# Kernel optimization log

Measured on AMD Instinct MI355X. Metric: run time of the kernel, lower is better.

Reference implementation:

```python
import jax, jax.numpy as jnp
import numpy as np

B, CQ, CKV, H, W = 8, 128, 64, 64, 64
DIM = CQ // 8  # qk_reduction=8 -> 16


def conv1x1(x, w, b):
    # x: [B, Cin, H, W], w: [Cout, Cin], b: [Cout]
    return jnp.einsum('bchw,oc->bohw', x, w) + b[None, :, None, None]


def setup_inputs() -> dict:
    key = jax.random.key(0)
    ks = jax.random.split(key, 12)
    s = 0.05
    return {
        'x4q': jax.random.normal(ks[0], (B, CQ, H, W), jnp.float32),
        'x4kv': jax.random.normal(ks[1], (B, CKV, H, W), jnp.float32),
        'Wq': jax.random.normal(ks[2], (DIM, CQ), jnp.float32) * s,
        'bq': jax.random.normal(ks[3], (DIM,), jnp.float32) * s,
        'Wk': jax.random.normal(ks[4], (DIM, CKV), jnp.float32) * s,
        'bk': jax.random.normal(ks[5], (DIM,), jnp.float32) * s,
        'Wv': jax.random.normal(ks[6], (CQ, CKV), jnp.float32) * s,
        'bv': jax.random.normal(ks[7], (CQ,), jnp.float32) * s,
        'Wo': jax.random.normal(ks[8], (CQ, CQ), jnp.float32) * s,
        'bo': jax.random.normal(ks[9], (CQ,), jnp.float32) * s,
        'gamma': jax.random.normal(ks[10], (1,), jnp.float32) * s,
    }


def reference(x4q, x4kv, Wq, bq, Wk, bk, Wv, bv, Wo, bo, gamma):
    q = conv1x1(x4q, Wq, bq)    # [B, DIM, H, W]
    k = conv1x1(x4kv, Wk, bk)   # [B, DIM, H, W]
    v = conv1x1(x4kv, Wv, bv)   # [B, CQ,  H, W]
    b, dim, h_, w_ = q.shape
    n = h_ * w_
    qf = q.reshape(b, dim, n)
    kf = k.reshape(b, dim, n)
    vf = v.reshape(b, -1, n)
    # score[b, n_query, m_key] = q^T k, scaled by dim^-0.5
    score = jnp.einsum('bdn,bdm->bnm', qf, kf) * (float(dim) ** -0.5)
    attention = jax.nn.softmax(score, axis=2)          # over keys m
    hmat = jnp.einsum('bcm,bnm->bcn', vf, attention)   # bmm(v, att^T)
    hmap = hmat.reshape(b, -1, h_, w_)
    hmap = conv1x1(hmap, Wo, bo)
    return gamma * hmap + x4q
```

## Files before the change

kernel.cpp:

```cpp
#include <hip/hip_runtime.h>

#define NB 8
#define CQ 128
#define CKV 64
#define NPIX 4096
#define QDIM 16
#define KVBLK 128
#define NTI (NPIX / KVBLK)

typedef float f32x4 __attribute__((ext_vector_type(4)));
typedef float f32x16 __attribute__((ext_vector_type(16)));
typedef __bf16 bf16x8 __attribute__((ext_vector_type(8)));
typedef unsigned short u16;
typedef u16 u16x4 __attribute__((ext_vector_type(4)));
typedef u16 u16x8 __attribute__((ext_vector_type(8)));
typedef unsigned int u32;
typedef u32 u32x2 __attribute__((ext_vector_type(2)));
typedef u32 u32x4 __attribute__((ext_vector_type(4)));

static __device__ __forceinline__ u16 f2bf(float f) {
  unsigned int u = __builtin_bit_cast(unsigned int, f);
  u = (u + 0x7FFFu + ((u >> 16) & 1u)) >> 16;
  return (u16)u;
}
static __device__ __forceinline__ u32 cvtpk(float lo, float hi) {
  u32 r; asm("v_cvt_pk_bf16_f32 %0, %1, %2" : "=v"(r) : "v"(lo), "v"(hi)); return r;
}
static __device__ __forceinline__ void plswap(u32& a, u32& b) {
#if __has_builtin(__builtin_amdgcn_permlane32_swap)
  u32x2 r = __builtin_amdgcn_permlane32_swap(a, b, false, false);
  a = r[0]; b = r[1];
#else
  asm volatile("v_permlane32_swap_b32 %0, %1" : "+v"(a), "+v"(b));
#endif
}
static __device__ __forceinline__ void gload_lds16(const void* g, void* l) {
  __builtin_amdgcn_global_load_lds((const __attribute__((address_space(1))) void*)g,
                                   (__attribute__((address_space(3))) void*)l, 16, 0, 0);
}

__global__ __launch_bounds__(256) void proj_qkv(
    const float* __restrict__ xq, const float* __restrict__ Wq, const float* __restrict__ bq,
    const float* __restrict__ xkv, const float* __restrict__ Wk, const float* __restrict__ bk,
    const float* __restrict__ Wv, const float* __restrict__ bv,
    u16* __restrict__ Qs, u16* __restrict__ Ks, u16* __restrict__ Vt)
{
  __shared__ __align__(16) char smem[50688];
  int t = threadIdx.x;
  if ((int)blockIdx.x < NB * 64) {
    int bid = (int)blockIdx.x;
    float (*wq)[CQ]        = (float(*)[CQ])smem;
    float (*wk)[CKV]       = (float(*)[CKV])(smem + 8192);
    float (*redq)[64][17]  = (float(*)[64][17])(smem + 12288);
    float (*redk)[64][17]  = (float(*)[64][17])(smem + 29696);
    for (int i = t; i < QDIM * CQ; i += 256) wq[i >> 7][i & 127] = Wq[i];
    for (int i = t; i < QDIM * CKV; i += 256) wk[i >> 6][i & 63] = Wk[i];
    __syncthreads();
    int b = bid >> 6;
    int n0 = (bid & 63) << 6;
    int px = t & 63, cg = t >> 6;
    int n = n0 + px;
    const float* xqp = xq + (size_t)b * CQ * NPIX + n;
    const float* xkp = xkv + (size_t)b * CKV * NPIX + n;
    float qa[QDIM], ka[QDIM];
    #pragma unroll
    for (int d = 0; d < QDIM; d++) { qa[d] = 0.f; ka[d] = 0.f; }
    int cq0 = cg * 32, ck0 = cg * 16;
    #pragma unroll 4
    for (int c = cq0; c < cq0 + 32; c++) {
      float x = xqp[(size_t)c * NPIX];
      #pragma unroll
      for (int d = 0; d < QDIM; d++) qa[d] = fmaf(wq[d][c], x, qa[d]);
    }
    #pragma unroll 4
    for (int c = ck0; c < ck0 + 16; c++) {
      float x = xkp[(size_t)c * NPIX];
      #pragma unroll
      for (int d = 0; d < QDIM; d++) ka[d] = fmaf(wk[d][c], x, ka[d]);
    }
    #pragma unroll
    for (int d = 0; d < QDIM; d++) { redq[cg][px][d] = qa[d]; redk[cg][px][d] = ka[d]; }
    __syncthreads();
    const float SC = 0.25f * 1.44269504088896340736f;
    int d0 = cg * 4;
    u16x4 oq, ok;
    #pragma unroll
    for (int j = 0; j < 4; j++) {
      float sq = redq[0][px][d0 + j] + redq[1][px][d0 + j]
               + redq[2][px][d0 + j] + redq[3][px][d0 + j] + bq[d0 + j];
      oq[j] = f2bf(sq * SC);
      float sk = redk[0][px][d0 + j] + redk[1][px][d0 + j]
               + redk[2][px][d0 + j] + redk[3][px][d0 + j] + bk[d0 + j];
      ok[j] = f2bf(sk);
    }
    size_t o = ((size_t)b * NPIX + n) * QDIM + d0;
    *(u16x4*)(Qs + o) = oq;
    *(u16x4*)(Ks + o) = ok;
  } else {
    int bid = (int)blockIdx.x - NB * 64;
    float (*wv)[CKV + 1] = (float(*)[CKV + 1])smem;
    float (*xs)[64 + 4]  = (float(*)[64 + 4])(smem + 33280);
    int b = bid >> 6;
    int n0 = (bid & 63) << 6;
    for (int i = t; i < CQ * CKV; i += 256) wv[i >> 6][i & 63] = Wv[i];
    const float* xp = xkv + (size_t)b * CKV * NPIX + n0;
    for (int i = t; i < CKV * 16; i += 256) {
      int c = i >> 4, c4 = (i & 15) * 4;
      *(f32x4*)(&xs[c][c4]) = *(const f32x4*)(xp + (size_t)c * NPIX + c4);
    }
    __syncthreads();
    int cog = t >> 4, pg = t & 15;
    int co0 = cog * 8, p0 = pg * 4;
    float acc[8][4];
    #pragma unroll
    for (int j = 0; j < 8; j++) {
      float bb = bv[co0 + j];
      #pragma unroll
      for (int p = 0; p < 4; p++) acc[j][p] = bb;
    }
    #pragma unroll 2
    for (int c = 0; c < CKV; c++) {
      float xv[4];
      #pragma unroll
      for (int p = 0; p < 4; p++) xv[p] = xs[c][p0 + p];
      #pragma unroll
      for (int j = 0; j < 8; j++) {
        float wvv = wv[co0 + j][c];
        #pragma unroll
        for (int p = 0; p < 4; p++) acc[j][p] = fmaf(wvv, xv[p], acc[j][p]);
      }
    }
    #pragma unroll
    for (int j = 0; j < 8; j++) {
      u16x4 ov;
      #pragma unroll
      for (int p = 0; p < 4; p++) ov[p] = f2bf(acc[j][p]);
      *(u16x4*)(Vt + ((size_t)b * CQ + co0 + j) * NPIX + n0 + p0) = ov;
    }
  }
}

__global__ __launch_bounds__(256, 2) void attn(
    const u16* __restrict__ Qs, const u16* __restrict__ Ks, const u16* __restrict__ Vt,
    const float* __restrict__ Wo, const float* __restrict__ bo,
    const float* __restrict__ gamma, const float* __restrict__ xq,
    float* __restrict__ out)
{
  __shared__ u16 v_s[2][128][128];
  __shared__ float d_red[2][2][32];
  __shared__ float d_x[2][32];
  __shared__ float d_inv[2][32];
  __shared__ float bos[128];

  int t = (int)threadIdx.x;
  int w = t >> 6, l = t & 63, l31 = l & 31, hi = l >> 5;
  int ph = w;
  int sw = ((int)blockIdx.x & 7) * 64 + ((int)blockIdx.x >> 3);
  int b = sw >> 6, q0 = (sw & 63) * 64;

  const u16* Qb = Qs + (size_t)b * NPIX * QDIM;
  const u16* Kb = Ks + (size_t)b * NPIX * QDIM;
  const u16* Vb = Vt + (size_t)b * CQ * NPIX;

  if (t < 128) bos[t] = bo[t];

  bf16x8 qf0 = *(const bf16x8*)(Qb + (size_t)(q0 + l31) * QDIM + hi * 8);
  bf16x8 qf1 = *(const bf16x8*)(Qb + (size_t)(q0 + 32 + l31) * QDIM + hi * 8);

  int row0 = w * 32 + (l >> 4);
  int lx = (l & 15) ^ (l >> 4);
  const u16* kp = Kb + (size_t)(ph * 32 + l31) * QDIM + hi * 8;
  int rsw = l31 & 15;

  f32x16 acc0[4], acc1[4];
  #pragma unroll
  for (int cb = 0; cb < 4; cb++)
    #pragma unroll
    for (int r = 0; r < 16; r++) { acc0[cb][r] = 0.f; acc1[cb][r] = 0.f; }
  float lsum0 = 0.f, lsum1 = 0.f;

  u32x4 afw0[2], afw1[2];

  auto PACK = [&](const f32x16& s, u32x4* aw, float& ls) {
    float pv[16];
    #pragma unroll
    for (int r = 0; r < 16; r++) {
      pv[r] = __builtin_amdgcn_exp2f(s[r]);
      ls += pv[r];
    }
    u32 a0 = cvtpk(pv[0], pv[1]),  b0 = cvtpk(pv[2], pv[3]);
    u32 c0 = cvtpk(pv[4], pv[5]),  d0 = cvtpk(pv[6], pv[7]);
    plswap(a0, c0); plswap(b0, d0);
    aw[0] = u32x4{a0, b0, c0, d0};
    u32 a1 = cvtpk(pv[8], pv[9]),  b1 = cvtpk(pv[10], pv[11]);
    u32 c1 = cvtpk(pv[12], pv[13]), d1 = cvtpk(pv[14], pv[15]);
    plswap(a1, c1); plswap(b1, d1);
    aw[1] = u32x4{a1, b1, c1, d1};
  };

  f32x16 z;
  #pragma unroll
  for (int r = 0; r < 16; r++) z[r] = 0.f;

  #pragma unroll
  for (int j = 0; j < 8; j++)
    gload_lds16(Vb + (size_t)(row0 + j * 4) * NPIX + (lx ^ ((j & 3) << 2)) * 8,
                &v_s[0][w * 32 + j * 4][0]);
  bf16x8 kc = *(const bf16x8*)(kp);
  bf16x8 kn = *(const bf16x8*)(kp + (size_t)KVBLK * QDIM);

  #pragma unroll 1
  for (int it = 0; it < NTI; it++) {
    __syncthreads();

    if (it + 1 < NTI) {
      #pragma unroll
      for (int j = 0; j < 8; j++)
        gload_lds16(Vb + (size_t)(row0 + j * 4) * NPIX + (lx ^ ((j & 3) << 2)) * 8
                       + (size_t)(it + 1) * KVBLK,
                    &v_s[(it + 1) & 1][w * 32 + j * 4][0]);
    }

    f32x16 s0 = __builtin_amdgcn_mfma_f32_32x32x16_bf16(kc, qf0, z, 0, 0, 0);
    f32x16 s1 = __builtin_amdgcn_mfma_f32_32x32x16_bf16(kc, qf1, z, 0, 0, 0);
    kc = kn;
    if (it + 2 < NTI) kn = *(const bf16x8*)(kp + (size_t)(it + 2) * KVBLK * QDIM);
    PACK(s0, afw0, lsum0);
    PACK(s1, afw1, lsum1);

    const u16 (*vs)[128] = v_s[it & 1];
    #pragma unroll
    for (int c = 0; c < 2; c++) {
      bf16x8 af0 = __builtin_bit_cast(bf16x8, afw0[c]);
      bf16x8 af1 = __builtin_bit_cast(bf16x8, afw1[c]);
      #pragma unroll
      for (int cb = 0; cb < 4; cb++) {
        int chunk = (ph * 4 + c * 2 + hi) ^ rsw;
        bf16x8 vf = *(const bf16x8*)(&vs[cb * 32 + l31][chunk * 8]);
        acc0[cb] = __builtin_amdgcn_mfma_f32_32x32x16_bf16(af0, vf, acc0[cb], 0, 0, 0);
        acc1[cb] = __builtin_amdgcn_mfma_f32_32x32x16_bf16(af1, vf, acc1[cb], 0, 0, 0);
      }
    }
  }

  float tot0 = lsum0 + __shfl_xor(lsum0, 32);
  float tot1 = lsum1 + __shfl_xor(lsum1, 32);

  __syncthreads();
  float* red = (float*)v_s;
  if (ph >= 2) {
    if (hi == 0) { d_red[ph - 2][0][l31] = tot0; d_red[ph - 2][1][l31] = tot1; }
    float* dst = red + (size_t)(ph - 2) * 64 * 128;
    #pragma unroll
    for (int cb = 0; cb < 4; cb++)
      #pragma unroll
      for (int r = 0; r < 16; r++) {
        int row = (r & 3) + 8 * (r >> 2) + 4 * hi;
        dst[(size_t)row * 128 + cb * 32 + l31] = acc0[cb][r];
        dst[(size_t)(row + 32) * 128 + cb * 32 + l31] = acc1[cb][r];
      }
  }
  __syncthreads();
  if (ph < 2) {
    tot0 += d_red[ph][0][l31];
    tot1 += d_red[ph][1][l31];
    const float* src = red + (size_t)ph * 64 * 128;
    #pragma unroll
    for (int cb = 0; cb < 4; cb++)
      #pragma unroll
      for (int r = 0; r < 16; r++) {
        int row = (r & 3) + 8 * (r >> 2) + 4 * hi;
        acc0[cb][r] += src[(size_t)row * 128 + cb * 32 + l31];
        acc1[cb][r] += src[(size_t)(row + 32) * 128 + cb * 32 + l31];
      }
    if (ph == 0) {
      if (hi == 0) d_x[0][l31] = tot1;
      #pragma unroll
      for (int cb = 0; cb < 4; cb++)
        #pragma unroll
        for (int r = 0; r < 16; r++) {
          int row = (r & 3) + 8 * (r >> 2) + 4 * hi;
          red[(size_t)(row + 32) * 128 + cb * 32 + l31] = acc1[cb][r];
        }
    } else {
      if (hi == 0) d_x[1][l31] = tot0;
      #pragma unroll
      for (int cb = 0; cb < 4; cb++)
        #pragma unroll
        for (int r = 0; r < 16; r++) {
          int row = (r & 3) + 8 * (r >> 2) + 4 * hi;
          red[8192 + (size_t)row * 128 + cb * 32 + l31] = acc0[cb][r];
        }
    }
  }
  __syncthreads();
  if (ph == 0) {
    float denom = tot0 + d_x[1][l31];
    if (hi == 0) d_inv[0][l31] = 1.0f / denom;
    #pragma unroll
    for (int cb = 0; cb < 4; cb++)
      #pragma unroll
      for (int r = 0; r < 16; r++) {
        int row = (r & 3) + 8 * (r >> 2) + 4 * hi;
        acc0[cb][r] += red[8192 + (size_t)row * 128 + cb * 32 + l31];
      }
  } else if (ph == 1) {
    float denom = tot1 + d_x[0][l31];
    if (hi == 0) d_inv[1][l31] = 1.0f / denom;
    #pragma unroll
    for (int cb = 0; cb < 4; cb++)
      #pragma unroll
      for (int r = 0; r < 16; r++) {
        int row = (r & 3) + 8 * (r >> 2) + 4 * hi;
        acc1[cb][r] += red[(size_t)(row + 32) * 128 + cb * 32 + l31];
      }
  }
  __syncthreads();
  u16* Old = (u16*)v_s;
  if (ph == 0) {
    #pragma unroll
    for (int cb = 0; cb < 4; cb++)
      #pragma unroll
      for (int r = 0; r < 16; r++) {
        int row = (r & 3) + 8 * (r >> 2) + 4 * hi;
        int c = cb * 32 + l31;
        Old[row * 128 + (((c >> 3) ^ (row & 15)) << 3) + (c & 7)] =
            f2bf(acc0[cb][r] * d_inv[0][row]);
      }
  } else if (ph == 1) {
    #pragma unroll
    for (int cb = 0; cb < 4; cb++)
      #pragma unroll
      for (int r = 0; r < 16; r++) {
        int q = 32 + (r & 3) + 8 * (r >> 2) + 4 * hi;
        int c = cb * 32 + l31;
        Old[q * 128 + (((c >> 3) ^ (q & 15)) << 3) + (c & 7)] =
            f2bf(acc1[cb][r] * d_inv[1][(q - 32)]);
      }
  }
  __syncthreads();
  bf16x8 woF[8];
  {
    const float* wrow = Wo + (size_t)(w * 32 + l31) * CQ + hi * 8;
    #pragma unroll
    for (int kc8 = 0; kc8 < 8; kc8++) {
      f32x4 a = *(const f32x4*)(wrow + kc8 * 16);
      f32x4 c4 = *(const f32x4*)(wrow + kc8 * 16 + 4);
      u32x4 pk = { cvtpk(a[0], a[1]), cvtpk(a[2], a[3]),
                   cvtpk(c4[0], c4[1]), cvtpk(c4[2], c4[3]) };
      woF[kc8] = __builtin_bit_cast(bf16x8, pk);
    }
  }
  float g = gamma[0];
  const float* xb = xq + (size_t)b * CQ * NPIX;
  float* ob = out + (size_t)b * CQ * NPIX;
  #pragma unroll
  for (int qb = 0; qb < 2; qb++) {
    f32x16 e = z;
    int q = qb * 32 + l31;
    #pragma unroll
    for (int kc8 = 0; kc8 < 8; kc8++) {
      int phys = (kc8 * 2 + hi) ^ (l31 & 15);
      bf16x8 of = *(const bf16x8*)(Old + q * 128 + phys * 8);
      e = __builtin_amdgcn_mfma_f32_32x32x16_bf16(woF[kc8], of, e, 0, 0, 0);
    }
    #pragma unroll
    for (int r = 0; r < 16; r++) {
      int o = w * 32 + (r & 3) + 8 * (r >> 2) + 4 * hi;
      size_t idx = (size_t)o * NPIX + q0 + qb * 32 + l31;
      ob[idx] = g * (e[r] + bos[o]) + xb[idx];
    }
  }
}

extern "C" void kernel_launch(void* const* d_in, const int* in_sizes, int n_in,
                              void* d_out, int out_size, void* d_ws, size_t ws_size,
                              hipStream_t stream) {
  const float* x4q  = (const float*)d_in[0];
  const float* x4kv = (const float*)d_in[1];
  const float* Wq   = (const float*)d_in[2];
  const float* bq   = (const float*)d_in[3];
  const float* Wk   = (const float*)d_in[4];
  const float* bk   = (const float*)d_in[5];
  const float* Wv   = (const float*)d_in[6];
  const float* bv   = (const float*)d_in[7];
  const float* Wo   = (const float*)d_in[8];
  const float* bo   = (const float*)d_in[9];
  const float* gamma = (const float*)d_in[10];
  float* out = (float*)d_out;

  u16* Qs = (u16*)d_ws;
  u16* Ks = Qs + (size_t)NB * NPIX * QDIM;
  u16* Vt = Ks + (size_t)NB * NPIX * QDIM;

  proj_qkv<<<dim3(NB * 128), dim3(256), 0, stream>>>(x4q, Wq, bq, x4kv, Wk, bk,
                                                     Wv, bv, Qs, Ks, Vt);
  attn<<<dim3(NB * 64), dim3(256), 0, stream>>>(Qs, Ks, Vt, Wo, bo, gamma, x4q, out);
}
```

Before: 77.31 us.

## Split attention block into 8 waves, one 32-query half per wave group

The attention kernel moves from 256 to 512 threads per block. Each wave now handles a single 32-query half instead of both halves, which halves the accumulator registers per wave and spreads the V tile load across twice as many threads. The cross-wave reduction is rewritten as a two-stage tree per query half, and the output projection gives one 32x32 tile to each wave. This raises the number of waves per CU to hide latency, at the cost of an extra barrier and more LDS traffic during the reduction.

After: 80.99 us. 4.8% more time.

```diff
diff --git a/kernel.cpp b/kernel.cpp
--- a/kernel.cpp
+++ b/kernel.cpp
@@ -13,7 +13,6 @@
 typedef __bf16 bf16x8 __attribute__((ext_vector_type(8)));
 typedef unsigned short u16;
 typedef u16 u16x4 __attribute__((ext_vector_type(4)));
-typedef u16 u16x8 __attribute__((ext_vector_type(8)));
 typedef unsigned int u32;
 typedef u32 u32x2 __attribute__((ext_vector_type(2)));
 typedef u32 u32x4 __attribute__((ext_vector_type(4)));
@@ -140,7 +139,7 @@
   }
 }
 
-__global__ __launch_bounds__(256, 2) void attn(
+__global__ __launch_bounds__(512, 4) void attn(
     const u16* __restrict__ Qs, const u16* __restrict__ Ks, const u16* __restrict__ Vt,
     const float* __restrict__ Wo, const float* __restrict__ bo,
     const float* __restrict__ gamma, const float* __restrict__ xq,
@@ -148,13 +147,12 @@
 {
   __shared__ u16 v_s[2][128][128];
   __shared__ float d_red[2][2][32];
-  __shared__ float d_x[2][32];
   __shared__ float d_inv[2][32];
   __shared__ float bos[128];
 
   int t = (int)threadIdx.x;
   int w = t >> 6, l = t & 63, l31 = l & 31, hi = l >> 5;
-  int ph = w;
+  int p = w >> 2, ph = w & 3;
   int sw = ((int)blockIdx.x & 7) * 64 + ((int)blockIdx.x >> 3);
   int b = sw >> 6, q0 = (sw & 63) * 64;
 
@@ -164,155 +162,123 @@
 
   if (t < 128) bos[t] = bo[t];
 
-  bf16x8 qf0 = *(const bf16x8*)(Qb + (size_t)(q0 + l31) * QDIM + hi * 8);
-  bf16x8 qf1 = *(const bf16x8*)(Qb + (size_t)(q0 + 32 + l31) * QDIM + hi * 8);
-
-  int row0 = w * 32 + (l >> 4);
+  bf16x8 qf = *(const bf16x8*)(Qb + (size_t)(q0 + p * 32 + l31) * QDIM + hi * 8);
+
+  int row0 = w * 16 + (l >> 4);
   int lx = (l & 15) ^ (l >> 4);
   const u16* kp = Kb + (size_t)(ph * 32 + l31) * QDIM + hi * 8;
   int rsw = l31 & 15;
 
-  f32x16 acc0[4], acc1[4];
+  f32x16 acc[4];
   #pragma unroll
   for (int cb = 0; cb < 4; cb++)
     #pragma unroll
-    for (int r = 0; r < 16; r++) { acc0[cb][r] = 0.f; acc1[cb][r] = 0.f; }
-  float lsum0 = 0.f, lsum1 = 0.f;
-
-  u32x4 afw0[2], afw1[2];
-
-  auto PACK = [&](const f32x16& s, u32x4* aw, float& ls) {
+    for (int r = 0; r < 16; r++) acc[cb][r] = 0.f;
+  float lsum = 0.f;
+
+  f32x16 z;
+  #pragma unroll
+  for (int r = 0; r < 16; r++) z[r] = 0.f;
+
+  #pragma unroll
+  for (int j = 0; j < 4; j++)
+    gload_lds16(Vb + (size_t)(row0 + j * 4) * NPIX + (lx ^ (j << 2)) * 8,
+                &v_s[0][w * 16 + j * 4][0]);
+  bf16x8 kc = *(const bf16x8*)(kp);
+  bf16x8 kn = *(const bf16x8*)(kp + (size_t)KVBLK * QDIM);
+
+  #pragma unroll 1
+  for (int it = 0; it < NTI; it++) {
+    __syncthreads();
+
+    if (it + 1 < NTI) {
+      #pragma unroll
+      for (int j = 0; j < 4; j++)
+        gload_lds16(Vb + (size_t)(row0 + j * 4) * NPIX + (lx ^ (j << 2)) * 8
+                       + (size_t)(it + 1) * KVBLK,
+                    &v_s[(it + 1) & 1][w * 16 + j * 4][0]);
+    }
+
+    f32x16 s = __builtin_amdgcn_mfma_f32_32x32x16_bf16(kc, qf, z, 0, 0, 0);
+    kc = kn;
+    if (it + 2 < NTI) kn = *(const bf16x8*)(kp + (size_t)(it + 2) * KVBLK * QDIM);
+
     float pv[16];
     #pragma unroll
     for (int r = 0; r < 16; r++) {
       pv[r] = __builtin_amdgcn_exp2f(s[r]);
-      ls += pv[r];
+      lsum += pv[r];
     }
     u32 a0 = cvtpk(pv[0], pv[1]),  b0 = cvtpk(pv[2], pv[3]);
     u32 c0 = cvtpk(pv[4], pv[5]),  d0 = cvtpk(pv[6], pv[7]);
     plswap(a0, c0); plswap(b0, d0);
-    aw[0] = u32x4{a0, b0, c0, d0};
     u32 a1 = cvtpk(pv[8], pv[9]),  b1 = cvtpk(pv[10], pv[11]);
     u32 c1 = cvtpk(pv[12], pv[13]), d1 = cvtpk(pv[14], pv[15]);
     plswap(a1, c1); plswap(b1, d1);
-    aw[1] = u32x4{a1, b1, c1, d1};
-  };
-
-  f32x16 z;
-  #pragma unroll
-  for (int r = 0; r < 16; r++) z[r] = 0.f;
-
-  #pragma unroll
-  for (int j = 0; j < 8; j++)
-    gload_lds16(Vb + (size_t)(row0 + j * 4) * NPIX + (lx ^ ((j & 3) << 2)) * 8,
-                &v_s[0][w * 32 + j * 4][0]);
-  bf16x8 kc = *(const bf16x8*)(kp);
-  bf16x8 kn = *(const bf16x8*)(kp + (size_t)KVBLK * QDIM);
-
-  #pragma unroll 1
-  for (int it = 0; it < NTI; it++) {
-    __syncthreads();
-
-    if (it + 1 < NTI) {
-      #pragma unroll
-      for (int j = 0; j < 8; j++)
-        gload_lds16(Vb + (size_t)(row0 + j * 4) * NPIX + (lx ^ ((j & 3) << 2)) * 8
-                       + (size_t)(it + 1) * KVBLK,
-                    &v_s[(it + 1) & 1][w * 32 + j * 4][0]);
-    }
-
-    f32x16 s0 = __builtin_amdgcn_mfma_f32_32x32x16_bf16(kc, qf0, z, 0, 0, 0);
-    f32x16 s1 = __builtin_amdgcn_mfma_f32_32x32x16_bf16(kc, qf1, z, 0, 0, 0);
-    kc = kn;
-    if (it + 2 < NTI) kn = *(const bf16x8*)(kp + (size_t)(it + 2) * KVBLK * QDIM);
-    PACK(s0, afw0, lsum0);
-    PACK(s1, afw1, lsum1);
+    u32x4 afw[2] = { {a0, b0, c0, d0}, {a1, b1, c1, d1} };
 
     const u16 (*vs)[128] = v_s[it & 1];
     #pragma unroll
     for (int c = 0; c < 2; c++) {
-      bf16x8 af0 = __builtin_bit_cast(bf16x8, afw0[c]);
-      bf16x8 af1 = __builtin_bit_cast(bf16x8, afw1[c]);
+      bf16x8 af = __builtin_bit_cast(bf16x8, afw[c]);
       #pragma unroll
       for (int cb = 0; cb < 4; cb++) {
         int chunk = (ph * 4 + c * 2 + hi) ^ rsw;
         bf16x8 vf = *(const bf16x8*)(&vs[cb * 32 + l31][chunk * 8]);
-        acc0[cb] = __builtin_amdgcn_mfma_f32_32x32x16_bf16(af0, vf, acc0[cb], 0, 0, 0);
-        acc1[cb] = __builtin_amdgcn_mfma_f32_32x32x16_bf16(af1, vf, acc1[cb], 0, 0, 0);
-      }
-    }
-  }
-
-  float tot0 = lsum0 + __shfl_xor(lsum0, 32);
-  float tot1 = lsum1 + __shfl_xor(lsum1, 32);
-
+        acc[cb] = __builtin_amdgcn_mfma_f32_32x32x16_bf16(af, vf, acc[cb], 0, 0, 0);
+      }
+    }
+  }
+
+  float tot = lsum + __shfl_xor(lsum, 32);
   __syncthreads();
   float* red = (float*)v_s;
   if (ph >= 2) {
-    if (hi == 0) { d_red[ph - 2][0][l31] = tot0; d_red[ph - 2][1][l31] = tot1; }
-    float* dst = red + (size_t)(ph - 2) * 64 * 128;
-    #pragma unroll
-    for (int cb = 0; cb < 4; cb++)
-      #pragma unroll
-      for (int r = 0; r < 16; r++) {
-        int row = (r & 3) + 8 * (r >> 2) + 4 * hi;
-        dst[(size_t)row * 128 + cb * 32 + l31] = acc0[cb][r];
-        dst[(size_t)(row + 32) * 128 + cb * 32 + l31] = acc1[cb][r];
+    if (hi == 0) d_red[p][ph - 2][l31] = tot;
+    float* dst = red + (((size_t)p * 2 + (ph - 2)) * 32) * 128;
+    #pragma unroll
+    for (int cb = 0; cb < 4; cb++)
+      #pragma unroll
+      for (int r = 0; r < 16; r++) {
+        int row = (r & 3) + 8 * (r >> 2) + 4 * hi;
+        dst[(size_t)row * 128 + cb * 32 + l31] = acc[cb][r];
       }
   }
   __syncthreads();
   if (ph < 2) {
-    tot0 += d_red[ph][0][l31];
-    tot1 += d_red[ph][1][l31];
-    const float* src = red + (size_t)ph * 64 * 128;
-    #pragma unroll
-    for (int cb = 0; cb < 4; cb++)
-      #pragma unroll
-      for (int r = 0; r < 16; r++) {
-        int row = (r & 3) + 8 * (r >> 2) + 4 * hi;
-        acc0[cb][r] += src[(size_t)row * 128 + cb * 32 + l31];
-        acc1[cb][r] += src[(size_t)(row + 32) * 128 + cb * 32 + l31];
-      }
-    if (ph == 0) {
-      if (hi == 0) d_x[0][l31] = tot1;
-      #pragma unroll
-      for (int cb = 0; cb < 4; cb++)
-        #pragma unroll
-        for (int r = 0; r < 16; r++) {
-          int row = (r & 3) + 8 * (r >> 2) + 4 * hi;
-          red[(size_t)(row + 32) * 128 + cb * 32 + l31] = acc1[cb][r];
-        }
-    } else {
-      if (hi == 0) d_x[1][l31] = tot0;
-      #pragma unroll
-      for (int cb = 0; cb < 4; cb++)
-        #pragma unroll
-        for (int r = 0; r < 16; r++) {
-          int row = (r & 3) + 8 * (r >> 2) + 4 * hi;
-          red[8192 + (size_t)row * 128 + cb * 32 + l31] = acc0[cb][r];
-        }
-    }
+    tot += d_red[p][ph][l31];
+    const float* src = red + (((size_t)p * 2 + ph) * 32) * 128;
+    #pragma unroll
+    for (int cb = 0; cb < 4; cb++)
+      #pragma unroll
+      for (int r = 0; r < 16; r++) {
+        int row = (r & 3) + 8 * (r >> 2) + 4 * hi;
+        acc[cb][r] += src[(size_t)row * 128 + cb * 32 + l31];
+      }
+  }
+  __syncthreads();
+  if (ph == 1) {
+    if (hi == 0) d_red[p][0][l31] = tot;
+    float* dst = red + ((size_t)p * 2 * 32) * 128;
+    #pragma unroll
+    for (int cb = 0; cb < 4; cb++)
+      #pragma unroll
+      for (int r = 0; r < 16; r++) {
+        int row = (r & 3) + 8 * (r >> 2) + 4 * hi;
+        dst[(size_t)row * 128 + cb * 32 + l31] = acc[cb][r];
+      }
   }
   __syncthreads();
   if (ph == 0) {
-    float denom = tot0 + d_x[1][l31];
-    if (hi == 0) d_inv[0][l31] = 1.0f / denom;
-    #pragma unroll
-    for (int cb = 0; cb < 4; cb++)
-      #pragma unroll
-      for (int r = 0; r < 16; r++) {
-        int row = (r & 3) + 8 * (r >> 2) + 4 * hi;
-        acc0[cb][r] += red[8192 + (size_t)row * 128 + cb * 32 + l31];
-      }
-  } else if (ph == 1) {
-    float denom = tot1 + d_x[0][l31];
-    if (hi == 0) d_inv[1][l31] = 1.0f / denom;
-    #pragma unroll
-    for (int cb = 0; cb < 4; cb++)
-      #pragma unroll
-      for (int r = 0; r < 16; r++) {
-        int row = (r & 3) + 8 * (r >> 2) + 4 * hi;
-        acc1[cb][r] += red[(size_t)(row + 32) * 128 + cb * 32 + l31];
+    tot += d_red[p][0][l31];
+    if (hi == 0) d_inv[p][l31] = 1.0f / tot;
+    const float* src = red + ((size_t)p * 2 * 32) * 128;
+    #pragma unroll
+    for (int cb = 0; cb < 4; cb++)
+      #pragma unroll
+      for (int r = 0; r < 16; r++) {
+        int row = (r & 3) + 8 * (r >> 2) + 4 * hi;
+        acc[cb][r] += src[(size_t)row * 128 + cb * 32 + l31];
       }
   }
   __syncthreads();
@@ -323,25 +289,17 @@
       #pragma unroll
       for (int r = 0; r < 16; r++) {
         int row = (r & 3) + 8 * (r >> 2) + 4 * hi;
+        int q = p * 32 + row;
         int c = cb * 32 + l31;
-        Old[row * 128 + (((c >> 3) ^ (row & 15)) << 3) + (c & 7)] =
-            f2bf(acc0[cb][r] * d_inv[0][row]);
-      }
-  } else if (ph == 1) {
-    #pragma unroll
-    for (int cb = 0; cb < 4; cb++)
-      #pragma unroll
-      for (int r = 0; r < 16; r++) {
-        int q = 32 + (r & 3) + 8 * (r >> 2) + 4 * hi;
-        int c = cb * 32 + l31;
-        Old[q * 128 + (((c >> 3) ^ (q & 15)) << 3) + (c & 7)] =
-            f2bf(acc1[cb][r] * d_inv[1][(q - 32)]);
-      }
-  }
-  __syncthreads();
+        Old[q * 128 + (((c >> 3) ^ (row & 15)) << 3) + (c & 7)] =
+            f2bf(acc[cb][r] * d_inv[p][row]);
+      }
+  }
+  __syncthreads();
+  int g2 = w >> 1, qh = w & 1;
   bf16x8 woF[8];
   {
-    const float* wrow = Wo + (size_t)(w * 32 + l31) * CQ + hi * 8;
+    const float* wrow = Wo + (size_t)(g2 * 32 + l31) * CQ + hi * 8;
     #pragma unroll
     for (int kc8 = 0; kc8 < 8; kc8++) {
       f32x4 a = *(const f32x4*)(wrow + kc8 * 16);
@@ -354,22 +312,19 @@
   float g = gamma[0];
   const float* xb = xq + (size_t)b * CQ * NPIX;
   float* ob = out + (size_t)b * CQ * NPIX;
-  #pragma unroll
-  for (int qb = 0; qb < 2; qb++) {
-    f32x16 e = z;
-    int q = qb * 32 + l31;
-    #pragma unroll
-    for (int kc8 = 0; kc8 < 8; kc8++) {
-      int phys = (kc8 * 2 + hi) ^ (l31 & 15);
-      bf16x8 of = *(const bf16x8*)(Old + q * 128 + phys * 8);
-      e = __builtin_amdgcn_mfma_f32_32x32x16_bf16(woF[kc8], of, e, 0, 0, 0);
-    }
-    #pragma unroll
-    for (int r = 0; r < 16; r++) {
-      int o = w * 32 + (r & 3) + 8 * (r >> 2) + 4 * hi;
-      size_t idx = (size_t)o * NPIX + q0 + qb * 32 + l31;
-      ob[idx] = g * (e[r] + bos[o]) + xb[idx];
-    }
+  f32x16 e = z;
+  int q = qh * 32 + l31;
+  #pragma unroll
+  for (int kc8 = 0; kc8 < 8; kc8++) {
+    int phys = (kc8 * 2 + hi) ^ (l31 & 15);
+    bf16x8 of = *(const bf16x8*)(Old + q * 128 + phys * 8);
+    e = __builtin_amdgcn_mfma_f32_32x32x16_bf16(woF[kc8], of, e, 0, 0, 0);
+  }
+  #pragma unroll
+  for (int r = 0; r < 16; r++) {
+    int o = g2 * 32 + (r & 3) + 8 * (r >> 2) + 4 * hi;
+    size_t idx = (size_t)o * NPIX + q0 + qh * 32 + l31;
+    ob[idx] = g * (e[r] + bos[o]) + xb[idx];
   }
 }
 
@@ -395,5 +350,5 @@
 
   proj_qkv<<<dim3(NB * 128), dim3(256), 0, stream>>>(x4q, Wq, bq, x4kv, Wk, bk,
                                                      Wv, bv, Qs, Ks, Vt);
-  attn<<<dim3(NB * 64), dim3(256), 0, stream>>>(Qs, Ks, Vt, Wo, bo, gamma, x4q, out);
-}
+  attn<<<dim3(NB * 64), dim3(512), 0, stream>>>(Qs, Ks, Vt, Wo, bo, gamma, x4q, out);
+}
```
